# Kernel optimization log

Measured on AMD Instinct MI355X. Metric: run time of the kernel, lower is better.

The kernel has to match this reference:

```python
import jax, jax.numpy as jnp
import numpy as np

D_MODEL = 1024
NUM_HEADS = 16
D_K = D_MODEL // NUM_HEADS
SCALE = float(np.sqrt(D_K))


def setup_inputs() -> dict:
    key = jax.random.key(0)
    ks = jax.random.split(key, 11)
    B, S, D = 2, 2048, D_MODEL
    def lin(kw):
        # xavier-uniform-ish weight, zero bias (matches torch init style)
        lim = float(np.sqrt(6.0 / (D + D)))
        return jax.random.uniform(kw, (D, D), jnp.float32, -lim, lim)
    return {
        "q": jax.random.normal(ks[0], (B, S, D), jnp.float32),
        "k": jax.random.normal(ks[1], (B, S, D), jnp.float32),
        "v": jax.random.normal(ks[2], (B, S, D), jnp.float32),
        "Wq": lin(ks[3]), "bq": jnp.zeros((D,), jnp.float32),
        "Wk": lin(ks[4]), "bk": jnp.zeros((D,), jnp.float32),
        "Wv": lin(ks[5]), "bv": jnp.zeros((D,), jnp.float32),
        "Wo": lin(ks[6]), "bo": jnp.zeros((D,), jnp.float32),
    }


def _split_heads(x):
    B, S, _ = x.shape
    return x.reshape(B, S, NUM_HEADS, D_K).transpose(0, 2, 1, 3)  # (B,H,S,dk)


def reference(q, k, v, Wq, bq, Wk, bk, Wv, bv, Wo, bo):
    # torch nn.Linear: y = x @ W.T + b
    Q = _split_heads(q @ Wq.T + bq)
    K = _split_heads(k @ Wk.T + bk)
    V = _split_heads(v @ Wv.T + bv)
    scores = jnp.einsum("bhqd,bhkd->bhqk", Q, K) / SCALE
    # numerically-stable softmax with detached max (as in the torch code)
    m = jax.lax.stop_gradient(jnp.max(scores, axis=-1, keepdims=True))
    exp_scores = jnp.exp(scores - m)
    attn = exp_scores / (jnp.sum(exp_scores, axis=-1, keepdims=True) + 1e-9)
    out = jnp.einsum("bhqk,bhkd->bhqd", attn, V)  # (B,H,S,dk)
    B, H, S, dk = out.shape
    out = out.transpose(0, 2, 1, 3).reshape(B, S, H * dk)
    return out @ Wo.T + bo
```

## Files before the change

kernel.cpp:

```cpp
#include <hip/hip_runtime.h>


#define D_MODEL 1024
#define NHEADS  16
#define DKH     64
#define SEQ     2048
#define BATCH   2
#define MTOT    (BATCH * SEQ)
#define XE      ((long)MTOT * D_MODEL)
#define WE      ((long)D_MODEL * D_MODEL)
#define QSCALE  0.18033688011112042f

typedef __attribute__((ext_vector_type(8)))  short short8v;
typedef __attribute__((ext_vector_type(4)))  short short4v;
typedef __attribute__((ext_vector_type(4)))  float f32x4;
typedef __attribute__((ext_vector_type(16))) float f32x16;

typedef __attribute__((address_space(1))) void as1_void;
typedef __attribute__((address_space(3))) void as3_void;

__device__ __forceinline__ void gload16(const void* g, void* l) {
    __builtin_amdgcn_global_load_lds((const as1_void*)g, (as3_void*)l, 16, 0, 0);
}

__device__ __forceinline__ unsigned short f2bf(float x) {
    unsigned int u = __float_as_uint(x);
    u += 0x7FFFu + ((u >> 16) & 1u);
    return (unsigned short)(u >> 16);
}

__device__ __forceinline__ float fexp2(float x) {
    return __builtin_amdgcn_exp2f(x);
}

__device__ __forceinline__ unsigned int cvt_pk_bf16(float lo, float hi) {
    unsigned int r;
    asm("v_cvt_pk_bf16_f32 %0, %1, %2" : "=v"(r) : "v"(lo), "v"(hi));
    return r;
}

__device__ __forceinline__ int swz_u(int row, int col) {
    int byte = (col << 1) ^ ((row & 7) << 4);
    return (row << 6) + (byte >> 1);
}

__device__ __forceinline__ int swz_v(int d, int kv) {
    int slot = (d & 6) | ((d >> 3) & 1);
    int byte = (kv << 1) ^ (slot << 4);
    return (d << 6) + (byte >> 1);
}

struct ConvArgs {
    const float*    src[7];
    unsigned short* dst[7];
    int             n4[7];
};

__global__ __launch_bounds__(256) void convert_kernel(ConvArgs a) {
    int z = blockIdx.y;
    const float4*   s = (const float4*)a.src[z];
    unsigned short* d = a.dst[z];
    int n = a.n4[z];
    for (int i = blockIdx.x * blockDim.x + threadIdx.x; i < n;
         i += gridDim.x * blockDim.x) {
        float4 v = s[i];
        ushort4 o;
        o.x = f2bf(v.x); o.y = f2bf(v.y); o.z = f2bf(v.z); o.w = f2bf(v.w);
        *(ushort4*)(d + 4L * i) = o;
    }
}

__device__ __forceinline__ void stv(float* p, float v)          { *p = v; }
__device__ __forceinline__ void stv(unsigned short* p, float v) { *p = f2bf(v); }

template <typename OutT>
__device__ __forceinline__ void gemm_core(const unsigned short* __restrict__ A,
                                          const unsigned short* __restrict__ Bm,
                                          const float* __restrict__ bias,
                                          OutT* __restrict__ C,
                                          int K, int N, float scale) {
    __shared__ unsigned short As[128 * 32];
    __shared__ unsigned short Bs[128 * 32];

    const int t    = threadIdx.x;
    const int lane = t & 63;
    const int w    = t >> 6;
    const int wm   = w >> 1, wn = w & 1;
    const int l15  = lane & 15, g = lane >> 4;
    const long m0  = (long)blockIdx.y * 128;
    const long n0  = (long)blockIdx.x * 128;

    f32x4 acc[4][4] = {};

    const int idx0 = t, idx1 = t + 256;
    const int r0 = idx0 >> 2, c0 = (idx0 & 3) * 8;
    const int r1 = idx1 >> 2, c1 = (idx1 & 3) * 8;
    const unsigned short* pa0 = A  + (m0 + r0) * K + c0;
    const unsigned short* pa1 = A  + (m0 + r1) * K + c1;
    const unsigned short* pb0 = Bm + (n0 + r0) * K + c0;
    const unsigned short* pb1 = Bm + (n0 + r1) * K + c1;

    for (int k0 = 0; k0 < K; k0 += 32) {
        gload16(pa0 + k0, &As[idx0 * 8]);
        gload16(pa1 + k0, &As[idx1 * 8]);
        gload16(pb0 + k0, &Bs[idx0 * 8]);
        gload16(pb1 + k0, &Bs[idx1 * 8]);
        __syncthreads();

        short8v af[4], bf_[4];
#pragma unroll
        for (int mf = 0; mf < 4; ++mf)
            af[mf] = *(const short8v*)&As[(wm * 64 + mf * 16 + l15) * 32 + g * 8];
#pragma unroll
        for (int nf = 0; nf < 4; ++nf)
            bf_[nf] = *(const short8v*)&Bs[(wn * 64 + nf * 16 + l15) * 32 + g * 8];
#pragma unroll
        for (int mf = 0; mf < 4; ++mf)
#pragma unroll
            for (int nf = 0; nf < 4; ++nf)
                acc[mf][nf] = __builtin_amdgcn_mfma_f32_16x16x32_bf16(
                    af[mf], bf_[nf], acc[mf][nf], 0, 0, 0);
        __syncthreads();
    }

    float bvv[4];
#pragma unroll
    for (int nf = 0; nf < 4; ++nf)
        bvv[nf] = bias[n0 + wn * 64 + nf * 16 + l15];

#pragma unroll
    for (int mf = 0; mf < 4; ++mf)
#pragma unroll
        for (int nf = 0; nf < 4; ++nf)
#pragma unroll
            for (int r = 0; r < 4; ++r) {
                long row = m0 + wm * 64 + mf * 16 + g * 4 + r;
                long col = n0 + wn * 64 + nf * 16 + l15;
                float v = (acc[mf][nf][r] + bvv[nf]) * scale;
                stv(C + row * (long)N + col, v);
            }
}

__global__ __launch_bounds__(256) void proj_kernel(
    const unsigned short* __restrict__ xb, const unsigned short* __restrict__ wb,
    const float* __restrict__ bq, const float* __restrict__ bk,
    const float* __restrict__ bv, unsigned short* __restrict__ qkv) {
    int z = blockIdx.z;
    const float* bias = (z == 0) ? bq : (z == 1) ? bk : bv;
    float scale = (z == 0) ? QSCALE : 1.0f;
    gemm_core<unsigned short>(xb + (long)z * XE, wb + (long)z * WE, bias,
                              qkv + (long)z * XE, D_MODEL, D_MODEL, scale);
}

__global__ __launch_bounds__(256) void out_kernel(
    const unsigned short* __restrict__ ob, const unsigned short* __restrict__ wo,
    const float* __restrict__ bo, float* __restrict__ out) {
    gemm_core<float>(ob, wo, bo, out, D_MODEL, D_MODEL, 1.0f);
}

#define KVB 4096

__global__ __launch_bounds__(256) void attn_kernel(
    const unsigned short* __restrict__ Qb, const unsigned short* __restrict__ Kb,
    const unsigned short* __restrict__ Vb, unsigned short* __restrict__ Ob) {
    __shared__ alignas(16) unsigned short Ks[2 * KVB];
    __shared__ alignas(16) unsigned short Vt[2 * KVB];
    __shared__ alignas(16) float corrS[4][32];

    const int t = threadIdx.x, lane = t & 63, w = t >> 6;
    const int l31 = lane & 31, h = lane >> 5;
    const int bh = blockIdx.y;
    const long headoff = (long)(bh >> 4) * SEQ * D_MODEL + (long)(bh & 15) * DKH;
    const int q0w = blockIdx.x * 128 + w * 32;

    short8v qf[4];
#pragma unroll
    for (int step = 0; step < 4; ++step)
        qf[step] = *(const short8v*)(Qb + headoff +
            (long)(q0w + l31) * D_MODEL + step * 16 + h * 8);

    short8v onesv;
#pragma unroll
    for (int j = 0; j < 8; ++j) onesv[j] = (short)0x3F80;

    f32x16 o[2] = {};
    f32x16 ol = {};
    float mrun = -3.0e38f;

    const int vd0  = (t & 31) * 2;
    const int vkv0 = (t >> 5) * 8;
    const int kr0 = t >> 3,         ks0  = t & 7;
    const int kr1 = (t + 256) >> 3, ks1_ = (t + 256) & 7;

    unsigned int va[8];

#define ISSUE_V(kt)                                                        \
    _Pragma("unroll")                                                      \
    for (int j = 0; j < 8; ++j)                                            \
        va[j] = *(const unsigned int*)(Vb + headoff +                      \
            (long)((kt) + vkv0 + j) * D_MODEL + vd0);

#define ISSUE_K(kt, off)                                                   \
    gload16(Kb + headoff + (long)((kt) + kr0) * D_MODEL +                  \
                ((ks0 ^ (kr0 & 7)) << 3), &Ks[(off) + t * 8]);             \
    gload16(Kb + headoff + (long)((kt) + kr1) * D_MODEL +                  \
                ((ks1_ ^ (kr1 & 7)) << 3), &Ks[(off) + (t + 256) * 8]);

#define WRITE_V(off)                                                       \
    {                                                                      \
        short8v ra, rb;                                                    \
        _Pragma("unroll")                                                  \
        for (int j = 0; j < 8; ++j) {                                      \
            ra[j] = (short)(va[j] & 0xffffu);                              \
            rb[j] = (short)(va[j] >> 16);                                  \
        }                                                                  \
        *(short8v*)&Vt[(off) + swz_v(vd0,     vkv0)] = ra;                 \
        *(short8v*)&Vt[(off) + swz_v(vd0 + 1, vkv0)] = rb;                 \
    }

    asm volatile("s_waitcnt vmcnt(0)" ::: "memory");
    ISSUE_V(0);
    ISSUE_K(0, 0);
    WRITE_V(0);
    int cur = 0;

    for (int it = 0; it < SEQ / 64; ++it) {
        const int nxt = cur ^ 1;
        const int ktn = ((it + 1) & (SEQ / 64 - 1)) * 64;
        ISSUE_V(ktn);
        ISSUE_K(ktn, nxt * KVB);
        asm volatile("s_waitcnt vmcnt(10)" ::: "memory");
        asm volatile("s_waitcnt lgkmcnt(0)" ::: "memory");
        __builtin_amdgcn_sched_barrier(0);
        __builtin_amdgcn_s_barrier();
        __builtin_amdgcn_sched_barrier(0);

        const int kO = cur * KVB;

        f32x16 st[2] = {};
        __builtin_amdgcn_s_setprio(1);
#pragma unroll
        for (int step = 0; step < 4; ++step) {
            short8v kf0 = *(const short8v*)&Ks[kO + swz_u(l31,      step * 16 + h * 8)];
            st[0] = __builtin_amdgcn_mfma_f32_32x32x16_bf16(kf0, qf[step], st[0], 0, 0, 0);
            short8v kf1 = *(const short8v*)&Ks[kO + swz_u(32 + l31, step * 16 + h * 8)];
            st[1] = __builtin_amdgcn_mfma_f32_32x32x16_bf16(kf1, qf[step], st[1], 0, 0, 0);
        }
        __builtin_amdgcn_s_setprio(0);

        float vmax = st[0][0];
#pragma unroll
        for (int b = 0; b < 2; ++b)
#pragma unroll
            for (int r = 0; r < 16; ++r)
                vmax = fmaxf(vmax, st[b][r]);
        vmax = fmaxf(vmax, __shfl_xor(vmax, 32));

        const bool grow = __any(vmax > mrun + 8.0f);
        if (grow) {
            float mnew = fmaxf(mrun, vmax);
            float corr = fexp2(mrun - mnew);
            mrun = mnew;
            if (lane < 32) corrS[w][l31] = corr;
        }

#pragma unroll
        for (int b = 0; b < 2; ++b)
#pragma unroll
            for (int r = 0; r < 16; ++r)
                st[b][r] = fexp2(st[b][r] - mrun);

        if (grow) {
#pragma unroll
            for (int q2 = 0; q2 < 4; ++q2) {
                float4 cv = *(const float4*)&corrS[w][q2 * 8 + h * 4];
#pragma unroll
                for (int r3 = 0; r3 < 4; ++r3) {
                    o[0][q2 * 4 + r3] *= cv[r3];
                    o[1][q2 * 4 + r3] *= cv[r3];
                    ol[q2 * 4 + r3]   *= cv[r3];
                }
            }
        }

        __builtin_amdgcn_s_setprio(1);
#pragma unroll
        for (int b = 0; b < 2; ++b)
#pragma unroll
            for (int s = 0; s < 2; ++s) {
                unsigned int u  = cvt_pk_bf16(st[b][s * 8 + 0], st[b][s * 8 + 1]);
                unsigned int u2 = cvt_pk_bf16(st[b][s * 8 + 2], st[b][s * 8 + 3]);
                unsigned int v  = cvt_pk_bf16(st[b][s * 8 + 4], st[b][s * 8 + 5]);
                unsigned int v2 = cvt_pk_bf16(st[b][s * 8 + 6], st[b][s * 8 + 7]);
                asm("v_permlane32_swap_b32 %0, %1" : "+v"(u),  "+v"(v));
                asm("v_permlane32_swap_b32 %0, %1" : "+v"(u2), "+v"(v2));
                uint4 pu = {u, u2, v, v2};
                short8v pa = __builtin_bit_cast(short8v, pu);
                ol = __builtin_amdgcn_mfma_f32_32x32x16_bf16(pa, onesv, ol, 0, 0, 0);
                short8v vb0 = *(const short8v*)&Vt[kO + swz_v(l31,      b * 32 + s * 16 + h * 8)];
                o[0] = __builtin_amdgcn_mfma_f32_32x32x16_bf16(pa, vb0, o[0], 0, 0, 0);
                short8v vb1 = *(const short8v*)&Vt[kO + swz_v(32 + l31, b * 32 + s * 16 + h * 8)];
                o[1] = __builtin_amdgcn_mfma_f32_32x32x16_bf16(pa, vb1, o[1], 0, 0, 0);
            }
        __builtin_amdgcn_s_setprio(0);

        WRITE_V(nxt * KVB);
        cur = nxt;
    }

#pragma unroll
    for (int q2 = 0; q2 < 4; ++q2)
#pragma unroll
        for (int r3 = 0; r3 < 4; ++r3) {
            float inv = 1.f / (ol[q2 * 4 + r3] + 1e-9f);
            long rowoff = headoff +
                (long)(q0w + q2 * 8 + h * 4 + r3) * D_MODEL;
            Ob[rowoff + l31]      = f2bf(o[0][q2 * 4 + r3] * inv);
            Ob[rowoff + 32 + l31] = f2bf(o[1][q2 * 4 + r3] * inv);
        }
#undef ISSUE_V
#undef ISSUE_K
#undef WRITE_V
}

extern "C" void kernel_launch(void* const* d_in, const int* in_sizes, int n_in,
                              void* d_out, int out_size, void* d_ws, size_t ws_size,
                              hipStream_t stream) {
    unsigned short* ws  = (unsigned short*)d_ws;
    unsigned short* xb  = ws;
    unsigned short* wb  = ws + 3L * XE;
    unsigned short* qkv = ws + 3L * XE + 4L * WE;
    unsigned short* ob  = qkv + 3L * XE;

    ConvArgs ca;
    ca.src[0] = (const float*)d_in[0]; ca.dst[0] = xb;           ca.n4[0] = (int)(XE / 4);
    ca.src[1] = (const float*)d_in[1]; ca.dst[1] = xb + XE;      ca.n4[1] = (int)(XE / 4);
    ca.src[2] = (const float*)d_in[2]; ca.dst[2] = xb + 2L * XE; ca.n4[2] = (int)(XE / 4);
    ca.src[3] = (const float*)d_in[3]; ca.dst[3] = wb;           ca.n4[3] = (int)(WE / 4);
    ca.src[4] = (const float*)d_in[5]; ca.dst[4] = wb + WE;      ca.n4[4] = (int)(WE / 4);
    ca.src[5] = (const float*)d_in[7]; ca.dst[5] = wb + 2L * WE; ca.n4[5] = (int)(WE / 4);
    ca.src[6] = (const float*)d_in[9]; ca.dst[6] = wb + 3L * WE; ca.n4[6] = (int)(WE / 4);

    hipLaunchKernelGGL(convert_kernel, dim3(512, 7), dim3(256), 0, stream, ca);

    hipLaunchKernelGGL(proj_kernel, dim3(8, 32, 3), dim3(256), 0, stream,
                       xb, wb, (const float*)d_in[4], (const float*)d_in[6],
                       (const float*)d_in[8], qkv);

    hipLaunchKernelGGL(attn_kernel, dim3(16, 32), dim3(256), 0, stream,
                       qkv, qkv + XE, qkv + 2L * XE, ob);

    hipLaunchKernelGGL(out_kernel, dim3(8, 32), dim3(256), 0, stream,
                       ob, wb + 3L * WE, (const float*)d_in[10], (float*)d_out);
}
```

Baseline: 143.5 us.

## Software-pipeline attention PV matmul one tile behind QK and softmax

The P·V MFMA block for the previous KV tile now runs right after the current tile's QK^T MFMAs, so matrix work overlaps with the exp/max softmax ALU work. The probabilities are kept in registers across iterations, and V moves to a triple-buffered LDS layout so the previous tile's V stays valid while the next one is written. The row-max reduction also becomes a tree instead of a serial chain. The cost is more LDS and more live registers, which could reduce occupancy or cause spills.

```diff
diff --git a/kernel.cpp b/kernel.cpp
--- a/kernel.cpp
+++ b/kernel.cpp
@@ -164,7 +164,7 @@
     const unsigned short* __restrict__ Qb, const unsigned short* __restrict__ Kb,
     const unsigned short* __restrict__ Vb, unsigned short* __restrict__ Ob) {
     __shared__ alignas(16) unsigned short Ks[2 * KVB];
-    __shared__ alignas(16) unsigned short Vt[2 * KVB];
+    __shared__ alignas(16) unsigned short Vt[3 * KVB];
     __shared__ alignas(16) float corrS[4][32];
 
     const int t = threadIdx.x, lane = t & 63, w = t >> 6;
@@ -186,6 +186,7 @@
     f32x16 o[2] = {};
     f32x16 ol = {};
     float mrun = -3.0e38f;
+    uint4 pa[4];
 
     const int vd0  = (t & 31) * 2;
     const int vkv0 = (t >> 5) * 8;
@@ -218,24 +219,47 @@
         *(short8v*)&Vt[(off) + swz_v(vd0 + 1, vkv0)] = rb;                 \
     }
 
+#define PV_BLOCK(vO)                                                       \
+    {                                                                      \
+        __builtin_amdgcn_s_setprio(1);                                     \
+        _Pragma("unroll")                                                  \
+        for (int b = 0; b < 2; ++b)                                        \
+            _Pragma("unroll")                                              \
+            for (int s = 0; s < 2; ++s) {                                  \
+                short8v pv_ = __builtin_bit_cast(short8v, pa[b * 2 + s]);  \
+                ol = __builtin_amdgcn_mfma_f32_32x32x16_bf16(              \
+                    pv_, onesv, ol, 0, 0, 0);                              \
+                short8v vb0 = *(const short8v*)&Vt[(vO) +                  \
+                    swz_v(l31,      b * 32 + s * 16 + h * 8)];             \
+                o[0] = __builtin_amdgcn_mfma_f32_32x32x16_bf16(            \
+                    pv_, vb0, o[0], 0, 0, 0);                              \
+                short8v vb1 = *(const short8v*)&Vt[(vO) +                  \
+                    swz_v(32 + l31, b * 32 + s * 16 + h * 8)];             \
+                o[1] = __builtin_amdgcn_mfma_f32_32x32x16_bf16(            \
+                    pv_, vb1, o[1], 0, 0, 0);                              \
+            }                                                              \
+        __builtin_amdgcn_s_setprio(0);                                     \
+    }
+
     asm volatile("s_waitcnt vmcnt(0)" ::: "memory");
     ISSUE_V(0);
     ISSUE_K(0, 0);
     WRITE_V(0);
-    int cur = 0;
+    int kcur = 0;
+    int vprev = 2, vcur = 0, vnxt = 1;
 
     for (int it = 0; it < SEQ / 64; ++it) {
-        const int nxt = cur ^ 1;
+        const int knxt = kcur ^ 1;
         const int ktn = ((it + 1) & (SEQ / 64 - 1)) * 64;
         ISSUE_V(ktn);
-        ISSUE_K(ktn, nxt * KVB);
+        ISSUE_K(ktn, knxt * KVB);
         asm volatile("s_waitcnt vmcnt(10)" ::: "memory");
         asm volatile("s_waitcnt lgkmcnt(0)" ::: "memory");
         __builtin_amdgcn_sched_barrier(0);
         __builtin_amdgcn_s_barrier();
         __builtin_amdgcn_sched_barrier(0);
 
-        const int kO = cur * KVB;
+        const int kO = kcur * KVB;
 
         f32x16 st[2] = {};
         __builtin_amdgcn_s_setprio(1);
@@ -248,12 +272,16 @@
         }
         __builtin_amdgcn_s_setprio(0);
 
-        float vmax = st[0][0];
-#pragma unroll
-        for (int b = 0; b < 2; ++b)
-#pragma unroll
-            for (int r = 0; r < 16; ++r)
-                vmax = fmaxf(vmax, st[b][r]);
+        if (it > 0) PV_BLOCK(vprev * KVB);
+
+        float m01[8];
+#pragma unroll
+        for (int j = 0; j < 8; ++j)
+            m01[j] = fmaxf(fmaxf(st[0][2 * j], st[0][2 * j + 1]),
+                           fmaxf(st[1][2 * j], st[1][2 * j + 1]));
+        float vmax = fmaxf(fmaxf(fmaxf(fmaxf(m01[0], m01[1]), m01[2]),
+                                 fmaxf(fmaxf(m01[3], m01[4]), m01[5])),
+                           fmaxf(m01[6], m01[7]));
         vmax = fmaxf(vmax, __shfl_xor(vmax, 32));
 
         const bool grow = __any(vmax > mrun + 8.0f);
@@ -262,15 +290,6 @@
             float corr = fexp2(mrun - mnew);
             mrun = mnew;
             if (lane < 32) corrS[w][l31] = corr;
-        }
-
-#pragma unroll
-        for (int b = 0; b < 2; ++b)
-#pragma unroll
-            for (int r = 0; r < 16; ++r)
-                st[b][r] = fexp2(st[b][r] - mrun);
-
-        if (grow) {
 #pragma unroll
             for (int q2 = 0; q2 < 4; ++q2) {
                 float4 cv = *(const float4*)&corrS[w][q2 * 8 + h * 4];
@@ -283,7 +302,12 @@
             }
         }
 
-        __builtin_amdgcn_s_setprio(1);
+#pragma unroll
+        for (int b = 0; b < 2; ++b)
+#pragma unroll
+            for (int r = 0; r < 16; ++r)
+                st[b][r] = fexp2(st[b][r] - mrun);
+
 #pragma unroll
         for (int b = 0; b < 2; ++b)
 #pragma unroll
@@ -294,20 +318,15 @@
                 unsigned int v2 = cvt_pk_bf16(st[b][s * 8 + 6], st[b][s * 8 + 7]);
                 asm("v_permlane32_swap_b32 %0, %1" : "+v"(u),  "+v"(v));
                 asm("v_permlane32_swap_b32 %0, %1" : "+v"(u2), "+v"(v2));
-                uint4 pu = {u, u2, v, v2};
-                short8v pa = __builtin_bit_cast(short8v, pu);
-                ol = __builtin_amdgcn_mfma_f32_32x32x16_bf16(pa, onesv, ol, 0, 0, 0);
-                short8v vb0 = *(const short8v*)&Vt[kO + swz_v(l31,      b * 32 + s * 16 + h * 8)];
-                o[0] = __builtin_amdgcn_mfma_f32_32x32x16_bf16(pa, vb0, o[0], 0, 0, 0);
-                short8v vb1 = *(const short8v*)&Vt[kO + swz_v(32 + l31, b * 32 + s * 16 + h * 8)];
-                o[1] = __builtin_amdgcn_mfma_f32_32x32x16_bf16(pa, vb1, o[1], 0, 0, 0);
+                pa[b * 2 + s] = (uint4){u, u2, v, v2};
             }
-        __builtin_amdgcn_s_setprio(0);
-
-        WRITE_V(nxt * KVB);
-        cur = nxt;
-    }
-
+
+        WRITE_V(vnxt * KVB);
+        kcur = knxt;
+        vprev = vcur; vcur = vnxt; vnxt = (vnxt == 2) ? 0 : vnxt + 1;
+    }
+
+    PV_BLOCK(vprev * KVB);
 #pragma unroll
     for (int q2 = 0; q2 < 4; ++q2)
 #pragma unroll
@@ -321,6 +340,7 @@
 #undef ISSUE_V
 #undef ISSUE_K
 #undef WRITE_V
+#undef PV_BLOCK
 }
 
 extern "C" void kernel_launch(void* const* d_in, const int* in_sizes, int n_in,
```

After: 143.0 us. About the same (-0.3%).

## Split attention KV sequence across two warp groups with in-block combine

Applied to the files above, without the earlier changes.

The attention block grows to 512 threads. Two groups of four waves each process alternate 64-key halves of a 128-key tile, so each group makes half as many loop iterations over the sequence. At the end, the per-group running maxima are exchanged through shared memory, partial outputs and row sums are rescaled and summed, and group 0 writes the result. This aims to increase wave-level parallelism and latency hiding per block, at the cost of more shared memory (about 66 KB), an extra combine phase with barriers, and possibly fewer blocks resident per CU. The rescale of prior accumulators is also moved before the exp step and the max reduction is rewritten as a tree.

```diff
diff --git a/kernel.cpp b/kernel.cpp
--- a/kernel.cpp
+++ b/kernel.cpp
@@ -158,20 +158,25 @@
     gemm_core<float>(ob, wo, bo, out, D_MODEL, D_MODEL, 1.0f);
 }
 
-#define KVB 4096
-
-__global__ __launch_bounds__(256) void attn_kernel(
+#define TSZ 4096
+#define NTS 16
+
+__global__ __launch_bounds__(512, 4) void attn_kernel(
     const unsigned short* __restrict__ Qb, const unsigned short* __restrict__ Kb,
     const unsigned short* __restrict__ Vb, unsigned short* __restrict__ Ob) {
-    __shared__ alignas(16) unsigned short Ks[2 * KVB];
-    __shared__ alignas(16) unsigned short Vt[2 * KVB];
-    __shared__ alignas(16) float corrS[4][32];
+    __shared__ alignas(16) unsigned char SM[67584];
+    unsigned short* KsB  = (unsigned short*)SM;
+    unsigned short* VtB  = (unsigned short*)(SM + 32768);
+    float*          corrS = (float*)(SM + 65536);
+    float*          mS    = (float*)(SM + 66560);
+    float*          comb  = (float*)SM;
 
     const int t = threadIdx.x, lane = t & 63, w = t >> 6;
     const int l31 = lane & 31, h = lane >> 5;
+    const int qg = w & 3, sp = w >> 2;
     const int bh = blockIdx.y;
     const long headoff = (long)(bh >> 4) * SEQ * D_MODEL + (long)(bh & 15) * DKH;
-    const int q0w = blockIdx.x * 128 + w * 32;
+    const int q0w = blockIdx.x * 128 + qg * 32;
 
     short8v qf[4];
 #pragma unroll
@@ -187,10 +192,10 @@
     f32x16 ol = {};
     float mrun = -3.0e38f;
 
-    const int vd0  = (t & 31) * 2;
-    const int vkv0 = (t >> 5) * 8;
-    const int kr0 = t >> 3,         ks0  = t & 7;
-    const int kr1 = (t + 256) >> 3, ks1_ = (t + 256) & 7;
+    const int vtile = t >> 8, t8 = t & 255;
+    const int vd0  = (t8 & 31) * 2;
+    const int vkv0 = (t8 >> 5) * 8;
+    const int kr0 = t >> 3, ks0 = t & 7;
 
     unsigned int va[8];
 
@@ -198,15 +203,17 @@
     _Pragma("unroll")                                                      \
     for (int j = 0; j < 8; ++j)                                            \
         va[j] = *(const unsigned int*)(Vb + headoff +                      \
-            (long)((kt) + vkv0 + j) * D_MODEL + vd0);
-
-#define ISSUE_K(kt, off)                                                   \
+            (long)((kt) + vtile * 64 + vkv0 + j) * D_MODEL + vd0);
+
+#define ISSUE_K(kt, dbuf)                                                  \
     gload16(Kb + headoff + (long)((kt) + kr0) * D_MODEL +                  \
-                ((ks0 ^ (kr0 & 7)) << 3), &Ks[(off) + t * 8]);             \
-    gload16(Kb + headoff + (long)((kt) + kr1) * D_MODEL +                  \
-                ((ks1_ ^ (kr1 & 7)) << 3), &Ks[(off) + (t + 256) * 8]);
-
-#define WRITE_V(off)                                                       \
+                ((ks0 ^ (kr0 & 7)) << 3),                                  \
+            &KsB[((dbuf) * 2 + 0) * TSZ + t * 8]);                         \
+    gload16(Kb + headoff + (long)((kt) + 64 + kr0) * D_MODEL +             \
+                ((ks0 ^ (kr0 & 7)) << 3),                                  \
+            &KsB[((dbuf) * 2 + 1) * TSZ + t * 8]);
+
+#define WRITE_V(dbuf)                                                      \
     {                                                                      \
         short8v ra, rb;                                                    \
         _Pragma("unroll")                                                  \
@@ -214,8 +221,9 @@
             ra[j] = (short)(va[j] & 0xffffu);                              \
             rb[j] = (short)(va[j] >> 16);                                  \
         }                                                                  \
-        *(short8v*)&Vt[(off) + swz_v(vd0,     vkv0)] = ra;                 \
-        *(short8v*)&Vt[(off) + swz_v(vd0 + 1, vkv0)] = rb;                 \
+        unsigned short* vt = &VtB[((dbuf) * 2 + vtile) * TSZ];             \
+        *(short8v*)&vt[swz_v(vd0,     vkv0)] = ra;                         \
+        *(short8v*)&vt[swz_v(vd0 + 1, vkv0)] = rb;                         \
     }
 
     asm volatile("s_waitcnt vmcnt(0)" ::: "memory");
@@ -224,36 +232,38 @@
     WRITE_V(0);
     int cur = 0;
 
-    for (int it = 0; it < SEQ / 64; ++it) {
+    for (int it = 0; it < NTS; ++it) {
         const int nxt = cur ^ 1;
-        const int ktn = ((it + 1) & (SEQ / 64 - 1)) * 64;
+        const int ktn = ((it + 1) & (NTS - 1)) * 128;
         ISSUE_V(ktn);
-        ISSUE_K(ktn, nxt * KVB);
+        ISSUE_K(ktn, nxt);
         asm volatile("s_waitcnt vmcnt(10)" ::: "memory");
         asm volatile("s_waitcnt lgkmcnt(0)" ::: "memory");
         __builtin_amdgcn_sched_barrier(0);
         __builtin_amdgcn_s_barrier();
         __builtin_amdgcn_sched_barrier(0);
 
-        const int kO = cur * KVB;
+        const int kO = (cur * 2 + sp) * TSZ;
 
         f32x16 st[2] = {};
         __builtin_amdgcn_s_setprio(1);
 #pragma unroll
         for (int step = 0; step < 4; ++step) {
-            short8v kf0 = *(const short8v*)&Ks[kO + swz_u(l31,      step * 16 + h * 8)];
+            short8v kf0 = *(const short8v*)&KsB[kO + swz_u(l31,      step * 16 + h * 8)];
             st[0] = __builtin_amdgcn_mfma_f32_32x32x16_bf16(kf0, qf[step], st[0], 0, 0, 0);
-            short8v kf1 = *(const short8v*)&Ks[kO + swz_u(32 + l31, step * 16 + h * 8)];
+            short8v kf1 = *(const short8v*)&KsB[kO + swz_u(32 + l31, step * 16 + h * 8)];
             st[1] = __builtin_amdgcn_mfma_f32_32x32x16_bf16(kf1, qf[step], st[1], 0, 0, 0);
         }
         __builtin_amdgcn_s_setprio(0);
 
-        float vmax = st[0][0];
-#pragma unroll
-        for (int b = 0; b < 2; ++b)
-#pragma unroll
-            for (int r = 0; r < 16; ++r)
-                vmax = fmaxf(vmax, st[b][r]);
+        float m01[8];
+#pragma unroll
+        for (int j = 0; j < 8; ++j)
+            m01[j] = fmaxf(fmaxf(st[0][2 * j], st[0][2 * j + 1]),
+                           fmaxf(st[1][2 * j], st[1][2 * j + 1]));
+        float vmax = fmaxf(fmaxf(fmaxf(fmaxf(m01[0], m01[1]), m01[2]),
+                                 fmaxf(fmaxf(m01[3], m01[4]), m01[5])),
+                           fmaxf(m01[6], m01[7]));
         vmax = fmaxf(vmax, __shfl_xor(vmax, 32));
 
         const bool grow = __any(vmax > mrun + 8.0f);
@@ -261,19 +271,10 @@
             float mnew = fmaxf(mrun, vmax);
             float corr = fexp2(mrun - mnew);
             mrun = mnew;
-            if (lane < 32) corrS[w][l31] = corr;
-        }
-
-#pragma unroll
-        for (int b = 0; b < 2; ++b)
-#pragma unroll
-            for (int r = 0; r < 16; ++r)
-                st[b][r] = fexp2(st[b][r] - mrun);
-
-        if (grow) {
+            if (lane < 32) corrS[w * 32 + l31] = corr;
 #pragma unroll
             for (int q2 = 0; q2 < 4; ++q2) {
-                float4 cv = *(const float4*)&corrS[w][q2 * 8 + h * 4];
+                float4 cv = *(const float4*)&corrS[w * 32 + q2 * 8 + h * 4];
 #pragma unroll
                 for (int r3 = 0; r3 < 4; ++r3) {
                     o[0][q2 * 4 + r3] *= cv[r3];
@@ -282,6 +283,12 @@
                 }
             }
         }
+
+#pragma unroll
+        for (int b = 0; b < 2; ++b)
+#pragma unroll
+            for (int r = 0; r < 16; ++r)
+                st[b][r] = fexp2(st[b][r] - mrun);
 
         __builtin_amdgcn_s_setprio(1);
 #pragma unroll
@@ -297,27 +304,64 @@
                 uint4 pu = {u, u2, v, v2};
                 short8v pa = __builtin_bit_cast(short8v, pu);
                 ol = __builtin_amdgcn_mfma_f32_32x32x16_bf16(pa, onesv, ol, 0, 0, 0);
-                short8v vb0 = *(const short8v*)&Vt[kO + swz_v(l31,      b * 32 + s * 16 + h * 8)];
+                short8v vb0 = *(const short8v*)&VtB[kO + swz_v(l31,      b * 32 + s * 16 + h * 8)];
                 o[0] = __builtin_amdgcn_mfma_f32_32x32x16_bf16(pa, vb0, o[0], 0, 0, 0);
-                short8v vb1 = *(const short8v*)&Vt[kO + swz_v(32 + l31, b * 32 + s * 16 + h * 8)];
+                short8v vb1 = *(const short8v*)&VtB[kO + swz_v(32 + l31, b * 32 + s * 16 + h * 8)];
                 o[1] = __builtin_amdgcn_mfma_f32_32x32x16_bf16(pa, vb1, o[1], 0, 0, 0);
             }
         __builtin_amdgcn_s_setprio(0);
 
-        WRITE_V(nxt * KVB);
+        WRITE_V(nxt);
         cur = nxt;
     }
 
-#pragma unroll
-    for (int q2 = 0; q2 < 4; ++q2)
+    asm volatile("s_waitcnt vmcnt(0)" ::: "memory");
+
+    if (lane < 32) mS[(sp * 4 + qg) * 32 + l31] = mrun;
+    __syncthreads();
+
+#pragma unroll
+    for (int q2 = 0; q2 < 4; ++q2) {
+        float4 ma = *(const float4*)&mS[(0 * 4 + qg) * 32 + q2 * 8 + h * 4];
+        float4 mb = *(const float4*)&mS[(1 * 4 + qg) * 32 + q2 * 8 + h * 4];
 #pragma unroll
         for (int r3 = 0; r3 < 4; ++r3) {
-            float inv = 1.f / (ol[q2 * 4 + r3] + 1e-9f);
-            long rowoff = headoff +
-                (long)(q0w + q2 * 8 + h * 4 + r3) * D_MODEL;
-            Ob[rowoff + l31]      = f2bf(o[0][q2 * 4 + r3] * inv);
-            Ob[rowoff + 32 + l31] = f2bf(o[1][q2 * 4 + r3] * inv);
-        }
+            float mt = fmaxf(ma[r3], mb[r3]);
+            float mo = (sp == 0) ? ma[r3] : mb[r3];
+            float sc = fexp2(mo - mt);
+            o[0][q2 * 4 + r3] *= sc;
+            o[1][q2 * 4 + r3] *= sc;
+            ol[q2 * 4 + r3]   *= sc;
+        }
+    }
+
+    if (sp == 1) {
+#pragma unroll
+        for (int c = 0; c < 16; ++c) {
+            comb[((c)      * 4 + qg) * 64 + lane] = o[0][c];
+            comb[((c + 16) * 4 + qg) * 64 + lane] = o[1][c];
+            comb[((c + 32) * 4 + qg) * 64 + lane] = ol[c];
+        }
+    }
+    __syncthreads();
+    if (sp == 0) {
+#pragma unroll
+        for (int c = 0; c < 16; ++c) {
+            o[0][c] += comb[((c)      * 4 + qg) * 64 + lane];
+            o[1][c] += comb[((c + 16) * 4 + qg) * 64 + lane];
+            ol[c]   += comb[((c + 32) * 4 + qg) * 64 + lane];
+        }
+#pragma unroll
+        for (int q2 = 0; q2 < 4; ++q2)
+#pragma unroll
+            for (int r3 = 0; r3 < 4; ++r3) {
+                float inv = 1.f / (ol[q2 * 4 + r3] + 1e-9f);
+                long rowoff = headoff +
+                    (long)(q0w + q2 * 8 + h * 4 + r3) * D_MODEL;
+                Ob[rowoff + l31]      = f2bf(o[0][q2 * 4 + r3] * inv);
+                Ob[rowoff + 32 + l31] = f2bf(o[1][q2 * 4 + r3] * inv);
+            }
+    }
 #undef ISSUE_V
 #undef ISSUE_K
 #undef WRITE_V
@@ -347,7 +391,7 @@
                        xb, wb, (const float*)d_in[4], (const float*)d_in[6],
                        (const float*)d_in[8], qkv);
 
-    hipLaunchKernelGGL(attn_kernel, dim3(16, 32), dim3(256), 0, stream,
+    hipLaunchKernelGGL(attn_kernel, dim3(16, 32), dim3(512), 0, stream,
                        qkv, qkv + XE, qkv + 2L * XE, ob);
 
     hipLaunchKernelGGL(out_kernel, dim3(8, 32), dim3(256), 0, stream,
```

Result: slower. 185.0 us (+28.9%).
